# Kernel optimization log

Measured on AMD Instinct MI355X. Metric: run time of the kernel, lower is better.

The kernel has to match this reference:

```python
import jax, jax.numpy as jnp
import numpy as np

N_NODES = 100000
N_FEAT = 128
N_EDGES = 640000
BATCH_SIZE = 50000


def setup_inputs() -> dict:
    key = jax.random.key(0)
    k1, k2 = jax.random.split(key)
    x = jax.random.normal(k1, (N_NODES, N_FEAT), dtype=jnp.float32)
    edge_index = jax.random.randint(k2, (2, N_EDGES), 0, N_NODES, dtype=jnp.int32)
    return {"x": x, "edge_index": edge_index, "batch_size": BATCH_SIZE}


def reference(x, edge_index, batch_size):
    # Filter edges whose destination is inside the target batch, then
    # scatter-sum source node features into destination rows (SpMM with a
    # 0/1 adjacency), matching adj.t().matmul(x) in the original.
    src = edge_index[0]
    dst = edge_index[1]
    valid = dst < batch_size                                  # [E]
    # Route invalid edges to a dummy segment (batch_size) and zero their values.
    seg = jnp.where(valid, dst, batch_size)                   # [E]
    vals = x[src] * valid[:, None].astype(x.dtype)            # [E, F] gather
    x_neighbors_sum = jax.ops.segment_sum(
        vals, seg, num_segments=batch_size + 1)[:batch_size]  # [B, F]
    node_labels = jnp.concatenate(
        [x[:batch_size, :], x_neighbors_sum], axis=-1)        # [B, 2F]
    return node_labels
```

## Files before the change

### kernel.cpp

```cpp
#include <hip/hip_runtime.h>

#define NFEAT 128
#define CAP 32
#define OVF_CAP 4096

typedef float vfloat4 __attribute__((ext_vector_type(4)));


__global__ void zero_kernel(int* __restrict__ p, int n) {
    int t = blockIdx.x * blockDim.x + threadIdx.x;
    if (t < n) p[t] = 0;
}

__global__ void bin_kernel(const int* __restrict__ src, const int* __restrict__ dst,
                           int* __restrict__ cnt, int* __restrict__ ovf_cnt,
                           int* __restrict__ ovf, int* __restrict__ bucket,
                           int E, int B) {
    int t = blockIdx.x * blockDim.x + threadIdx.x;
    int e0 = t << 2;
    if (e0 >= E) return;
    if (e0 + 4 <= E) {
        const int4 d4 = *(const int4*)(dst + e0);
        const int4 s4 = *(const int4*)(src + e0);
        int dd[4] = {d4.x, d4.y, d4.z, d4.w};
        int ss[4] = {s4.x, s4.y, s4.z, s4.w};
        #pragma unroll
        for (int i = 0; i < 4; ++i) {
            int d = dd[i];
            if (d >= B) continue;
            int pos = atomicAdd(&cnt[d], 1);
            if (pos < CAP) {
                bucket[d * CAP + pos] = ss[i];
            } else {
                int o = atomicAdd(ovf_cnt, 1);
                if (o < OVF_CAP) { ovf[2 * o] = ss[i]; ovf[2 * o + 1] = d; }
            }
        }
    } else {
        for (int e = e0; e < E; ++e) {
            int d = dst[e];
            if (d >= B) continue;
            int pos = atomicAdd(&cnt[d], 1);
            if (pos < CAP) {
                bucket[d * CAP + pos] = src[e];
            } else {
                int o = atomicAdd(ovf_cnt, 1);
                if (o < OVF_CAP) { ovf[2 * o] = src[e]; ovf[2 * o + 1] = d; }
            }
        }
    }
}

__global__ void aggregate_kernel(const float4* __restrict__ x4,
                                 const int* __restrict__ cnt,
                                 const int* __restrict__ bucket,
                                 float4* __restrict__ out4, int B) {
    int wv   = (blockIdx.x * blockDim.x + threadIdx.x) >> 6;
    int lane = threadIdx.x & 63;
    int h    = lane >> 5;
    int l    = lane & 31;
    int w0   = wv * 2;
    if (w0 >= B) return;
    int row   = w0 + h;
    bool rowok = row < B;

    int k = 0;
    if (rowok) { k = cnt[row]; if (k > CAP) k = CAP; }
    int sid = (l < k) ? bucket[(size_t)w0 * CAP + lane] : 0;
    float4 xd = rowok ? x4[(size_t)row * 32 + l] : make_float4(0.f, 0.f, 0.f, 0.f);

    int ko   = __shfl(k, lane ^ 32, 64);
    int kmax = k > ko ? k : ko;

    float4 acc = make_float4(0.f, 0.f, 0.f, 0.f);
    int hb = h << 5;
    int j = 0;
    for (; j + 4 <= kmax; j += 4) {
        int s0 = __shfl(sid, hb + j,     64);
        int s1 = __shfl(sid, hb + j + 1, 64);
        int s2 = __shfl(sid, hb + j + 2, 64);
        int s3 = __shfl(sid, hb + j + 3, 64);
        float4 v0 = x4[(size_t)s0 * 32 + l];
        float4 v1 = x4[(size_t)s1 * 32 + l];
        float4 v2 = x4[(size_t)s2 * 32 + l];
        float4 v3 = x4[(size_t)s3 * 32 + l];
        if (j + 1 <= k) { acc.x += v0.x; acc.y += v0.y; acc.z += v0.z; acc.w += v0.w; }
        if (j + 2 <= k) { acc.x += v1.x; acc.y += v1.y; acc.z += v1.z; acc.w += v1.w; }
        if (j + 3 <= k) { acc.x += v2.x; acc.y += v2.y; acc.z += v2.z; acc.w += v2.w; }
        if (j + 4 <= k) { acc.x += v3.x; acc.y += v3.y; acc.z += v3.z; acc.w += v3.w; }
    }
    for (; j < kmax; ++j) {
        int s = __shfl(sid, hb + j, 64);
        float4 v = x4[(size_t)s * 32 + l];
        if (j < k) { acc.x += v.x; acc.y += v.y; acc.z += v.z; acc.w += v.w; }
    }

    if (rowok) {
        size_t o = (size_t)row * 64;
        vfloat4 xdn  = {xd.x, xd.y, xd.z, xd.w};
        vfloat4 accn = {acc.x, acc.y, acc.z, acc.w};
        __builtin_nontemporal_store(xdn,  (vfloat4*)&out4[o + l]);
        __builtin_nontemporal_store(accn, (vfloat4*)&out4[o + 32 + l]);
    }
}

__global__ void ovf_apply_kernel(const float* __restrict__ x,
                                 const int* __restrict__ ovf_cnt,
                                 const int* __restrict__ ovf,
                                 float* __restrict__ out, int B) {
    int n = *ovf_cnt;
    if (n > OVF_CAP) n = OVF_CAP;
    int t = blockIdx.x * blockDim.x + threadIdx.x;
    int e = t >> 5;
    if (e >= n) return;
    int c = t & 31;
    int s = ovf[2 * e], d = ovf[2 * e + 1];
    const float4 v = ((const float4*)(x + (size_t)s * NFEAT))[c];
    float* o = out + (size_t)d * 256 + NFEAT + c * 4;
    unsafeAtomicAdd(o + 0, v.x);
    unsafeAtomicAdd(o + 1, v.y);
    unsafeAtomicAdd(o + 2, v.z);
    unsafeAtomicAdd(o + 3, v.w);
}

__global__ void hist_kernel(const int* __restrict__ dst, int* __restrict__ cnt,
                            int E, int B) {
    int e = blockIdx.x * blockDim.x + threadIdx.x;
    if (e >= E) return;
    int d = dst[e];
    if (d < B) atomicAdd(&cnt[d], 1);
}

__global__ void alloc_kernel(const int* __restrict__ cnt, int* __restrict__ off,
                             int* __restrict__ deg, int* __restrict__ cursor, int B) {
    int t = blockIdx.x * blockDim.x + threadIdx.x;
    int lane = threadIdx.x & 63;
    int c = (t < B) ? cnt[t] : 0;
    int v = c;
    #pragma unroll
    for (int d = 1; d < 64; d <<= 1) {
        int n = __shfl_up(v, d, 64);
        if (lane >= d) v += n;
    }
    int total = __shfl(v, 63, 64);
    int base = 0;
    if (lane == 63 && total > 0) base = atomicAdd(cursor, total);
    base = __shfl(base, 63, 64);
    if (t < B) { off[t] = base + v - c; deg[t] = c; }
}

__global__ void scatter_kernel(const int* __restrict__ src, const int* __restrict__ dst,
                               int* __restrict__ cnt, const int* __restrict__ off,
                               int* __restrict__ bucket, int E, int B) {
    int e = blockIdx.x * blockDim.x + threadIdx.x;
    if (e >= E) return;
    int d = dst[e];
    if (d >= B) return;
    int old = atomicSub(&cnt[d], 1);
    bucket[off[d] + old - 1] = src[e];
}

__global__ void aggregate_csr_kernel(const float2* __restrict__ x2,
                                     const int* __restrict__ off, const int* __restrict__ deg,
                                     const int* __restrict__ bucket,
                                     float2* __restrict__ out2, int B) {
    int w = (blockIdx.x * blockDim.x + threadIdx.x) >> 6;
    int lane = threadIdx.x & 63;
    if (w >= B) return;
    int base = off[w];
    int k = deg[w];
    float2 acc = make_float2(0.f, 0.f);
    for (int j = 0; j < k; ++j) {
        int s = bucket[base + j];
        float2 v = x2[(size_t)s * 64 + lane];
        acc.x += v.x; acc.y += v.y;
    }
    float2 xd = x2[(size_t)w * 64 + lane];
    size_t o = (size_t)w * 128;
    out2[o + lane] = xd;
    out2[o + 64 + lane] = acc;
}

extern "C" void kernel_launch(void* const* d_in, const int* in_sizes, int n_in,
                              void* d_out, int out_size, void* d_ws, size_t ws_size,
                              hipStream_t stream) {
    const float* x  = (const float*)d_in[0];
    const int*   ei = (const int*)d_in[1];
    const int E = in_sizes[1] / 2;
    const int B = out_size / (2 * NFEAT);
    float* out = (float*)d_out;
    const int* src = ei;
    const int* dst = ei + E;

    size_t need_bin = ((size_t)B * (CAP + 1) + 1 + 2 * OVF_CAP) * sizeof(int);
    size_t need_csr = ((size_t)3 * B + 1 + E) * sizeof(int);

    if (ws_size >= need_bin) {
        int* cnt     = (int*)d_ws;
        int* ovf_cnt = cnt + B;
        int* ovf     = ovf_cnt + 1;
        int* bucket  = ovf + 2 * OVF_CAP;

        int nz = B + 1;
        zero_kernel<<<(nz + 255) / 256, 256, 0, stream>>>(cnt, nz);
        int nbin_threads = (E + 3) / 4;
        bin_kernel<<<(nbin_threads + 255) / 256, 256, 0, stream>>>(
            src, dst, cnt, ovf_cnt, ovf, bucket, E, B);
        int npairs = (B + 1) / 2;
        aggregate_kernel<<<(npairs + 3) / 4, 256, 0, stream>>>(
            (const float4*)x, cnt, bucket, (float4*)out, B);
        ovf_apply_kernel<<<(OVF_CAP * 32 + 255) / 256, 256, 0, stream>>>(x, ovf_cnt, ovf, out, B);
    } else {
        int* cnt    = (int*)d_ws;
        int* off    = cnt + B;
        int* deg    = off + B;
        int* cursor = deg + B;
        int* bucket = cursor + 1;
        int nz = 3 * B + 1;
        zero_kernel<<<(nz + 255) / 256, 256, 0, stream>>>(cnt, nz);
        hist_kernel<<<(E + 255) / 256, 256, 0, stream>>>(dst, cnt, E, B);
        alloc_kernel<<<(B + 255) / 256, 256, 0, stream>>>(cnt, off, deg, cursor, B);
        scatter_kernel<<<(E + 255) / 256, 256, 0, stream>>>(src, dst, cnt, off, bucket, E, B);
        aggregate_csr_kernel<<<(B + 3) / 4, 256, 0, stream>>>(
            (const float2*)x, off, deg, bucket, (float2*)out, B);
    }
}
```

Baseline: 141.2 us.

## Fuse zero, bin, aggregate and overflow into one cooperative persistent kernel

Replaces the four separate launches (zero counters, bin edges, aggregate, overflow atomic apply) with a single cooperative kernel that uses grid-wide syncs between phases and grid-stride loops over 1024 blocks. Overflow edges are now folded into the aggregation loop by a linear scan of the overflow list, done only for rows whose count exceeds the cap, instead of a separate atomic-add kernel. The aim is to remove launch overhead and the inter-kernel gaps. In exchange it adds the cost of grid.sync, a fixed grid size that may not fill the device, and a serial overflow scan per overflowing row.

```diff
diff --git a/kernel.cpp b/kernel.cpp
--- a/kernel.cpp
+++ b/kernel.cpp
@@ -1,4 +1,7 @@
 #include <hip/hip_runtime.h>
+#include <hip/hip_cooperative_groups.h>
+
+namespace cg = cooperative_groups;
 
 #define NFEAT 128
 #define CAP 32
@@ -6,40 +9,42 @@
 
 typedef float vfloat4 __attribute__((ext_vector_type(4)));
 
-
-__global__ void zero_kernel(int* __restrict__ p, int n) {
-    int t = blockIdx.x * blockDim.x + threadIdx.x;
-    if (t < n) p[t] = 0;
-}
-
-__global__ void bin_kernel(const int* __restrict__ src, const int* __restrict__ dst,
-                           int* __restrict__ cnt, int* __restrict__ ovf_cnt,
-                           int* __restrict__ ovf, int* __restrict__ bucket,
-                           int E, int B) {
-    int t = blockIdx.x * blockDim.x + threadIdx.x;
-    int e0 = t << 2;
-    if (e0 >= E) return;
-    if (e0 + 4 <= E) {
-        const int4 d4 = *(const int4*)(dst + e0);
-        const int4 s4 = *(const int4*)(src + e0);
+__global__ void __launch_bounds__(256, 4) fused_kernel(
+    const float4* __restrict__ x4,
+    const int* __restrict__ src, const int* __restrict__ dst,
+    int* __restrict__ cnt, int* __restrict__ ovf_cnt, int* __restrict__ ovf,
+    int* __restrict__ bucket, float4* __restrict__ out4,
+    int E, int B)
+{
+    cg::grid_group grid = cg::this_grid();
+    const int t  = blockIdx.x * blockDim.x + threadIdx.x;
+    const int nt = gridDim.x * blockDim.x;
+
+    for (int i = t; i <= B; i += nt) cnt[i] = 0;
+    grid.sync();
+
+    const int nvec = E >> 2;
+    for (int i = t; i < nvec; i += nt) {
+        const int4 d4 = ((const int4*)dst)[i];
+        const int4 s4 = ((const int4*)src)[i];
         int dd[4] = {d4.x, d4.y, d4.z, d4.w};
         int ss[4] = {s4.x, s4.y, s4.z, s4.w};
         #pragma unroll
-        for (int i = 0; i < 4; ++i) {
-            int d = dd[i];
+        for (int u = 0; u < 4; ++u) {
+            int d = dd[u];
             if (d >= B) continue;
             int pos = atomicAdd(&cnt[d], 1);
             if (pos < CAP) {
-                bucket[d * CAP + pos] = ss[i];
+                bucket[d * CAP + pos] = ss[u];
             } else {
                 int o = atomicAdd(ovf_cnt, 1);
-                if (o < OVF_CAP) { ovf[2 * o] = ss[i]; ovf[2 * o + 1] = d; }
+                if (o < OVF_CAP) { ovf[2 * o] = ss[u]; ovf[2 * o + 1] = d; }
             }
         }
-    } else {
-        for (int e = e0; e < E; ++e) {
-            int d = dst[e];
-            if (d >= B) continue;
+    }
+    for (int e = (nvec << 2) + t; e < E; e += nt) {
+        int d = dst[e];
+        if (d < B) {
             int pos = atomicAdd(&cnt[d], 1);
             if (pos < CAP) {
                 bucket[d * CAP + pos] = src[e];
@@ -49,78 +54,73 @@
             }
         }
     }
-}
-
-__global__ void aggregate_kernel(const float4* __restrict__ x4,
-                                 const int* __restrict__ cnt,
-                                 const int* __restrict__ bucket,
-                                 float4* __restrict__ out4, int B) {
-    int wv   = (blockIdx.x * blockDim.x + threadIdx.x) >> 6;
-    int lane = threadIdx.x & 63;
-    int h    = lane >> 5;
-    int l    = lane & 31;
-    int w0   = wv * 2;
-    if (w0 >= B) return;
-    int row   = w0 + h;
-    bool rowok = row < B;
-
-    int k = 0;
-    if (rowok) { k = cnt[row]; if (k > CAP) k = CAP; }
-    int sid = (l < k) ? bucket[(size_t)w0 * CAP + lane] : 0;
-    float4 xd = rowok ? x4[(size_t)row * 32 + l] : make_float4(0.f, 0.f, 0.f, 0.f);
-
-    int ko   = __shfl(k, lane ^ 32, 64);
-    int kmax = k > ko ? k : ko;
-
-    float4 acc = make_float4(0.f, 0.f, 0.f, 0.f);
-    int hb = h << 5;
-    int j = 0;
-    for (; j + 4 <= kmax; j += 4) {
-        int s0 = __shfl(sid, hb + j,     64);
-        int s1 = __shfl(sid, hb + j + 1, 64);
-        int s2 = __shfl(sid, hb + j + 2, 64);
-        int s3 = __shfl(sid, hb + j + 3, 64);
-        float4 v0 = x4[(size_t)s0 * 32 + l];
-        float4 v1 = x4[(size_t)s1 * 32 + l];
-        float4 v2 = x4[(size_t)s2 * 32 + l];
-        float4 v3 = x4[(size_t)s3 * 32 + l];
-        if (j + 1 <= k) { acc.x += v0.x; acc.y += v0.y; acc.z += v0.z; acc.w += v0.w; }
-        if (j + 2 <= k) { acc.x += v1.x; acc.y += v1.y; acc.z += v1.z; acc.w += v1.w; }
-        if (j + 3 <= k) { acc.x += v2.x; acc.y += v2.y; acc.z += v2.z; acc.w += v2.w; }
-        if (j + 4 <= k) { acc.x += v3.x; acc.y += v3.y; acc.z += v3.z; acc.w += v3.w; }
-    }
-    for (; j < kmax; ++j) {
-        int s = __shfl(sid, hb + j, 64);
-        float4 v = x4[(size_t)s * 32 + l];
-        if (j < k) { acc.x += v.x; acc.y += v.y; acc.z += v.z; acc.w += v.w; }
-    }
-
-    if (rowok) {
-        size_t o = (size_t)row * 64;
-        vfloat4 xdn  = {xd.x, xd.y, xd.z, xd.w};
-        vfloat4 accn = {acc.x, acc.y, acc.z, acc.w};
-        __builtin_nontemporal_store(xdn,  (vfloat4*)&out4[o + l]);
-        __builtin_nontemporal_store(accn, (vfloat4*)&out4[o + 32 + l]);
-    }
-}
-
-__global__ void ovf_apply_kernel(const float* __restrict__ x,
-                                 const int* __restrict__ ovf_cnt,
-                                 const int* __restrict__ ovf,
-                                 float* __restrict__ out, int B) {
-    int n = *ovf_cnt;
-    if (n > OVF_CAP) n = OVF_CAP;
+    grid.sync();
+
+    const int wv   = t >> 6;
+    const int lane = t & 63;
+    const int nwv  = nt >> 6;
+    const int h    = lane >> 5;
+    const int l    = lane & 31;
+    const int hb   = h << 5;
+    int novf = *ovf_cnt;
+    if (novf > OVF_CAP) novf = OVF_CAP;
+
+    for (int pr = wv; 2 * pr < B; pr += nwv) {
+        int w0  = 2 * pr;
+        int row = w0 + h;
+        bool rowok = row < B;
+        int korig = rowok ? cnt[row] : 0;
+        int k = korig > CAP ? CAP : korig;
+        int sid = (l < k) ? bucket[(size_t)w0 * CAP + lane] : 0;
+        float4 xd = rowok ? x4[(size_t)row * 32 + l] : make_float4(0.f, 0.f, 0.f, 0.f);
+
+        int ko   = __shfl(k, lane ^ 32, 64);
+        int kmax = k > ko ? k : ko;
+
+        float4 acc = make_float4(0.f, 0.f, 0.f, 0.f);
+        int j = 0;
+        for (; j + 4 <= kmax; j += 4) {
+            int s0 = __shfl(sid, hb + j,     64);
+            int s1 = __shfl(sid, hb + j + 1, 64);
+            int s2 = __shfl(sid, hb + j + 2, 64);
+            int s3 = __shfl(sid, hb + j + 3, 64);
+            float4 v0 = x4[(size_t)s0 * 32 + l];
+            float4 v1 = x4[(size_t)s1 * 32 + l];
+            float4 v2 = x4[(size_t)s2 * 32 + l];
+            float4 v3 = x4[(size_t)s3 * 32 + l];
+            if (j + 1 <= k) { acc.x += v0.x; acc.y += v0.y; acc.z += v0.z; acc.w += v0.w; }
+            if (j + 2 <= k) { acc.x += v1.x; acc.y += v1.y; acc.z += v1.z; acc.w += v1.w; }
+            if (j + 3 <= k) { acc.x += v2.x; acc.y += v2.y; acc.z += v2.z; acc.w += v2.w; }
+            if (j + 4 <= k) { acc.x += v3.x; acc.y += v3.y; acc.z += v3.z; acc.w += v3.w; }
+        }
+        for (; j < kmax; ++j) {
+            int s = __shfl(sid, hb + j, 64);
+            float4 v = x4[(size_t)s * 32 + l];
+            if (j < k) { acc.x += v.x; acc.y += v.y; acc.z += v.z; acc.w += v.w; }
+        }
+
+        if (korig > CAP) {
+            for (int o = 0; o < novf; ++o) {
+                if (ovf[2 * o + 1] == row) {
+                    float4 v = x4[(size_t)ovf[2 * o] * 32 + l];
+                    acc.x += v.x; acc.y += v.y; acc.z += v.z; acc.w += v.w;
+                }
+            }
+        }
+
+        if (rowok) {
+            size_t o = (size_t)row * 64;
+            vfloat4 xdn  = {xd.x, xd.y, xd.z, xd.w};
+            vfloat4 accn = {acc.x, acc.y, acc.z, acc.w};
+            __builtin_nontemporal_store(xdn,  (vfloat4*)&out4[o + l]);
+            __builtin_nontemporal_store(accn, (vfloat4*)&out4[o + 32 + l]);
+        }
+    }
+}
+
+__global__ void zero_kernel(int* __restrict__ p, int n) {
     int t = blockIdx.x * blockDim.x + threadIdx.x;
-    int e = t >> 5;
-    if (e >= n) return;
-    int c = t & 31;
-    int s = ovf[2 * e], d = ovf[2 * e + 1];
-    const float4 v = ((const float4*)(x + (size_t)s * NFEAT))[c];
-    float* o = out + (size_t)d * 256 + NFEAT + c * 4;
-    unsafeAtomicAdd(o + 0, v.x);
-    unsafeAtomicAdd(o + 1, v.y);
-    unsafeAtomicAdd(o + 2, v.z);
-    unsafeAtomicAdd(o + 3, v.w);
+    if (t < n) p[t] = 0;
 }
 
 __global__ void hist_kernel(const int* __restrict__ dst, int* __restrict__ cnt,
@@ -193,7 +193,6 @@
     const int* dst = ei + E;
 
     size_t need_bin = ((size_t)B * (CAP + 1) + 1 + 2 * OVF_CAP) * sizeof(int);
-    size_t need_csr = ((size_t)3 * B + 1 + E) * sizeof(int);
 
     if (ws_size >= need_bin) {
         int* cnt     = (int*)d_ws;
@@ -201,15 +200,16 @@
         int* ovf     = ovf_cnt + 1;
         int* bucket  = ovf + 2 * OVF_CAP;
 
-        int nz = B + 1;
-        zero_kernel<<<(nz + 255) / 256, 256, 0, stream>>>(cnt, nz);
-        int nbin_threads = (E + 3) / 4;
-        bin_kernel<<<(nbin_threads + 255) / 256, 256, 0, stream>>>(
-            src, dst, cnt, ovf_cnt, ovf, bucket, E, B);
-        int npairs = (B + 1) / 2;
-        aggregate_kernel<<<(npairs + 3) / 4, 256, 0, stream>>>(
-            (const float4*)x, cnt, bucket, (float4*)out, B);
-        ovf_apply_kernel<<<(OVF_CAP * 32 + 255) / 256, 256, 0, stream>>>(x, ovf_cnt, ovf, out, B);
+        const float4* x4p = (const float4*)x;
+        float4* out4p = (float4*)out;
+        int Ea = E, Ba = B;
+        const int* srcp = src;
+        const int* dstp = dst;
+        void* args[] = { (void*)&x4p, (void*)&srcp, (void*)&dstp,
+                         (void*)&cnt, (void*)&ovf_cnt, (void*)&ovf,
+                         (void*)&bucket, (void*)&out4p, (void*)&Ea, (void*)&Ba };
+        hipLaunchCooperativeKernel((const void*)fused_kernel,
+                                   dim3(1024), dim3(256), args, 0, stream);
     } else {
         int* cnt    = (int*)d_ws;
         int* off    = cnt + B;
```

Measured after the change: 324.6 us. +129.9%, slower.
